# Kernel tuning notes

Hardware: AMD Instinct MI355X
Metric: run time of the kernel (lower is better)

Reference implementation:

```python
import jax, jax.numpy as jnp
import numpy as np

NUM_HEADS = 12

def rel_indices(N):
    # [N, N, 3] = (dx, dy, dist^2) between patches on an img x img grid
    img = int(N ** 0.5)
    ind = jnp.arange(img)[None, :] - jnp.arange(img)[:, None]      # [img, img]
    indx = jnp.tile(ind, (img, img))                               # [N, N]
    indy = jnp.repeat(jnp.repeat(ind, img, axis=0), img, axis=1)   # [N, N]
    indd = indx ** 2 + indy ** 2
    return jnp.stack([indx, indy, indd], axis=-1).astype(jnp.float32)

def setup_inputs() -> dict:
    key = jax.random.key(0)
    ks = jax.random.split(key, 8)
    B, N, C, H = 16, 576, 768, NUM_HEADS
    std = 0.02  # trunc_normal init scale in the original
    return {
        "x": jax.random.normal(ks[0], (B, N, C), jnp.float32),
        "w_qk": jax.random.normal(ks[1], (C, 2 * C), jnp.float32) * std,
        "w_v": jax.random.normal(ks[2], (C, C), jnp.float32) * std,
        "w_proj": jax.random.normal(ks[3], (C, C), jnp.float32) * std,
        "b_proj": jnp.zeros((C,), jnp.float32),
        "w_pos": jax.random.normal(ks[4], (3, H), jnp.float32) * std,
        "b_pos": jnp.zeros((H,), jnp.float32),
        "gating": jnp.ones((H,), jnp.float32),
    }

def reference(x, w_qk, w_v, w_proj, b_proj, w_pos, b_pos, gating):
    B, N, C = x.shape
    H = NUM_HEADS
    Dh = C // H
    scale = Dh ** -0.5

    # q, k: [B, H, N, Dh]
    qk = (x @ w_qk).reshape(B, N, 2, H, Dh)
    q = jnp.transpose(qk[:, :, 0], (0, 2, 1, 3))
    k = jnp.transpose(qk[:, :, 1], (0, 2, 1, 3))

    # content scores, softmax over keys
    patch_score = jax.nn.softmax(
        jnp.einsum("bhnd,bhmd->bhnm", q, k) * scale, axis=-1)

    # positional scores: rel_indices [N,N,3] -> [H,N,N], softmax over keys
    rel = rel_indices(N)
    pos_logits = jnp.einsum("nmk,kh->hnm", rel, w_pos) + b_pos[:, None, None]
    pos_score = jax.nn.softmax(pos_logits, axis=-1)  # [H, N, N]

    # sigmoid gating + renormalization
    g = jax.nn.sigmoid(gating)[None, :, None, None]
    attn = (1.0 - g) * patch_score + g * pos_score[None]
    attn = attn / jnp.sum(attn, axis=-1, keepdims=True)

    # v: [B, H, N, Dh]
    v = jnp.transpose((x @ w_v).reshape(B, N, H, Dh), (0, 2, 1, 3))

    out = jnp.einsum("bhnm,bhmd->bnhd", attn, v).reshape(B, N, C)
    out = out @ w_proj + b_proj
    return (out, attn, v)
```

## Files before the change

kernel.cpp:

```cpp
#include <hip/hip_runtime.h>
#include <hip/hip_bf16.h>

typedef __bf16 bf16;
typedef __attribute__((ext_vector_type(4))) __bf16 bf16x4;
typedef __attribute__((ext_vector_type(8))) __bf16 bf16x8;
typedef __attribute__((ext_vector_type(4))) float floatx4;

#define BB 16
#define NN 576
#define CC 768
#define HH 12
#define DH 64

#define GLOAD_LDS16(gp, lp) __builtin_amdgcn_global_load_lds( \
    (const __attribute__((address_space(1))) unsigned int*)(const void*)(gp), \
    (__attribute__((address_space(3))) unsigned int*)(void*)(lp), 16, 0, 0)

__global__ void k_convert(const float* __restrict__ in, bf16* __restrict__ out, int n4){
  int i = blockIdx.x*blockDim.x + threadIdx.x;
  if (i < n4){
    float4 f = ((const float4*)in)[i];
    bf16x4 o;
    o[0]=(bf16)f.x; o[1]=(bf16)f.y; o[2]=(bf16)f.z; o[3]=(bf16)f.w;
    ((bf16x4*)out)[i] = o;
  }
}

__global__ void k_transpose(const float* __restrict__ src, bf16* __restrict__ dst, int R, int Cc){
  __shared__ float tile[32][33];
  int c0 = blockIdx.x*32, r0 = blockIdx.y*32;
  int tx = threadIdx.x & 31, ty = threadIdx.x >> 5;
  #pragma unroll
  for (int i=0;i<4;i++)
    tile[ty + i*8][tx] = src[(size_t)(r0 + ty + i*8)*Cc + c0 + tx];
  __syncthreads();
  #pragma unroll
  for (int i=0;i<4;i++)
    dst[(size_t)(c0 + ty + i*8)*R + r0 + tx] = (bf16)tile[tx][ty + i*8];
}

__global__ __launch_bounds__(256) void k_pos(const float* __restrict__ w_pos, bf16* __restrict__ pos){
  int t = threadIdx.x, wv = t>>6, lane = t&63;
  int rowid = blockIdx.x*4 + wv;
  int h = rowid / NN, n = rowid % NN;
  float w0 = w_pos[h], w1 = w_pos[HH + h], w2 = w_pos[2*HH + h];
  int nx = n % 24, ny = n / 24;
  float e[9]; float mx = -1e30f;
  #pragma unroll
  for (int j=0;j<9;j++){
    int m = lane + 64*j;
    float dx = (float)(m % 24 - nx);
    float dy = (float)(m / 24 - ny);
    float l = dx*w0 + dy*w1 + (dx*dx + dy*dy)*w2;
    e[j] = l; mx = fmaxf(mx, l);
  }
  #pragma unroll
  for (int s=1;s<64;s<<=1) mx = fmaxf(mx, __shfl_xor(mx, s, 64));
  float sum = 0.f;
  #pragma unroll
  for (int j=0;j<9;j++){ e[j] = __expf(e[j]-mx); sum += e[j]; }
  #pragma unroll
  for (int s=1;s<64;s<<=1) sum += __shfl_xor(sum, s, 64);
  float inv = 1.f/sum;
  bf16* dst = pos + (size_t)rowid*NN;
  #pragma unroll
  for (int j=0;j<9;j++) dst[lane + 64*j] = (bf16)(e[j]*inv);
}

__device__ __forceinline__ void gemm128_main(
    const bf16* __restrict__ A, const bf16* __restrict__ B,
    int lda, int ldb, int K, bf16* As, bf16* Bs, floatx4 (*acc)[4])
{
  int t = threadIdx.x;
  int w = t>>6, m16 = t&15, q = (t&63)>>4;
  int wr = (w>>1)*64, wc = (w&1)*64;
  int sr = t>>2, kg = (t&3)*8;
  bf16* ldsA = As + w*512;
  bf16* ldsB = Bs + w*512;
  for (int k0 = 0; k0 < K; k0 += 32){
    GLOAD_LDS16(A + (size_t)sr*lda      + k0 + kg, ldsA);
    GLOAD_LDS16(A + (size_t)(sr+64)*lda + k0 + kg, ldsA + 2048);
    GLOAD_LDS16(B + (size_t)sr*ldb      + k0 + kg, ldsB);
    GLOAD_LDS16(B + (size_t)(sr+64)*ldb + k0 + kg, ldsB + 2048);
    __syncthreads();
    bf16x8 af[4], bfv[4];
    #pragma unroll
    for (int rt=0;rt<4;rt++) af[rt]  = *(const bf16x8*)&As[(wr + rt*16 + m16)*32 + q*8];
    #pragma unroll
    for (int ct=0;ct<4;ct++) bfv[ct] = *(const bf16x8*)&Bs[(wc + ct*16 + m16)*32 + q*8];
    #pragma unroll
    for (int rt=0;rt<4;rt++)
      #pragma unroll
      for (int ct=0;ct<4;ct++)
        acc[rt][ct] = __builtin_amdgcn_mfma_f32_16x16x32_bf16(af[rt], bfv[ct], acc[rt][ct], 0, 0, 0);
    __syncthreads();
  }
}

__global__ __launch_bounds__(256) void k_gemm1(
    const bf16* __restrict__ x_bf, const bf16* __restrict__ wcatT,
    bf16* __restrict__ q_bf, bf16* __restrict__ k_bf,
    bf16* __restrict__ vt_bf, float* __restrict__ v_out)
{
  __shared__ bf16 As[128*32];
  __shared__ bf16 Bs[128*32];
  int cb = blockIdx.x % 18, rb = blockIdx.x / 18;
  int rowBase = rb*128, colBase = cb*128;
  floatx4 zero = {0.f,0.f,0.f,0.f};
  floatx4 acc[4][4];
  #pragma unroll
  for (int a=0;a<4;a++)
    #pragma unroll
    for (int b=0;b<4;b++) acc[a][b] = zero;
  gemm128_main(x_bf + (size_t)rowBase*CC, wcatT + (size_t)colBase*CC, CC, CC, CC, As, Bs, acc);
  int t = threadIdx.x;
  int w = t>>6, m16 = t&15, q = (t&63)>>4;
  int wr = (w>>1)*64, wc = (w&1)*64;
  #pragma unroll
  for (int rt=0;rt<4;rt++){
    #pragma unroll
    for (int i=0;i<4;i++){
      int row = rowBase + wr + rt*16 + q*4 + i;
      int b = row / NN, n = row % NN;
      #pragma unroll
      for (int ct=0;ct<4;ct++){
        int col = colBase + wc + ct*16 + m16;
        float val = acc[rt][ct][i];
        if (col < 2*CC){
          int s = col / CC, rem = col % CC;
          int h = rem >> 6, d = rem & 63;
          bf16* dst = s ? k_bf : q_bf;
          float sv = s ? val : val*0.125f;
          dst[(((size_t)(b*HH + h)*NN + n) << 6) + d] = (bf16)sv;
        } else {
          int rem = col - 2*CC;
          int h = rem >> 6, d = rem & 63;
          v_out[(((size_t)(b*HH + h)*NN + n) << 6) + d] = val;
          vt_bf[((size_t)(b*HH + h)*DH + d)*NN + n] = (bf16)val;
        }
      }
    }
  }
}

__global__ __launch_bounds__(256, 2) void k_attn_pv(
    const bf16* __restrict__ q_bf, const bf16* __restrict__ k_bf,
    const bf16* __restrict__ vt_bf,
    const bf16* __restrict__ pos, const float* __restrict__ gating,
    float* __restrict__ attn_out, bf16* __restrict__ out1_bf)
{
  __shared__ __align__(16) char smem[64*1200];
  int qt = blockIdx.x % 9, bh = blockIdx.x / 9;
  int b = bh / HH, h = bh % HH;
  int n0 = qt*64;
  int t = threadIdx.x;
  int wv = t>>6, m16 = t&15, q = (t&63)>>4;

  const bf16* qrow = q_bf + ((size_t)bh*NN + n0 + wv*16 + m16)*DH;
  bf16x8 afr0 = *(const bf16x8*)&qrow[q*8];
  bf16x8 afr1 = *(const bf16x8*)&qrow[32 + q*8];

  const bf16* Kg = k_bf + (size_t)bh*NN*DH;
  floatx4 acc[36];
  #pragma unroll
  for (int T=0;T<36;T++) acc[T] = (floatx4){0.f,0.f,0.f,0.f};

  int key0 = t>>3, g16 = (t&7) ^ (key0 & 7);
  #pragma unroll
  for (int kt=0; kt<9; kt++){
    __syncthreads();
    const bf16* src0 = Kg + (size_t)(kt*64 + key0)*DH + g16*8;
    GLOAD_LDS16(src0,           smem + wv*1024);
    GLOAD_LDS16(src0 + 32*DH,   smem + 4096 + wv*1024);
    __syncthreads();
    #pragma unroll
    for (int ct=0; ct<4; ct++){
      int key = ct*16 + m16;
      int swz = key & 7;
      bf16x8 b0 = *(const bf16x8*)(smem + key*128 + ((q ^ swz)<<4));
      bf16x8 b1 = *(const bf16x8*)(smem + key*128 + (((4 + q) ^ swz)<<4));
      acc[kt*4+ct] = __builtin_amdgcn_mfma_f32_16x16x32_bf16(afr0, b0, acc[kt*4+ct], 0, 0, 0);
      acc[kt*4+ct] = __builtin_amdgcn_mfma_f32_16x16x32_bf16(afr1, b1, acc[kt*4+ct], 0, 0, 0);
    }
  }

  float mx[4], ps[4], bs[4];
  #pragma unroll
  for (int i=0;i<4;i++) mx[i] = -1e30f;
  #pragma unroll
  for (int T=0;T<36;T++)
    #pragma unroll
    for (int i=0;i<4;i++) mx[i] = fmaxf(mx[i], acc[T][i]);
  #pragma unroll
  for (int s=1;s<16;s<<=1)
    #pragma unroll
    for (int i=0;i<4;i++) mx[i] = fmaxf(mx[i], __shfl_xor(mx[i], s, 64));
  #pragma unroll
  for (int i=0;i<4;i++) ps[i] = 0.f;
  #pragma unroll
  for (int T=0;T<36;T++)
    #pragma unroll
    for (int i=0;i<4;i++){ float e = __expf(acc[T][i]-mx[i]); acc[T][i]=e; ps[i]+=e; }
  #pragma unroll
  for (int s=1;s<16;s<<=1)
    #pragma unroll
    for (int i=0;i<4;i++) ps[i] += __shfl_xor(ps[i], s, 64);

  float g = 1.f/(1.f + __expf(-gating[h]));
  float ig[4];
  #pragma unroll
  for (int i=0;i<4;i++){ ig[i] = (1.f-g)/ps[i]; bs[i] = 0.f; }

  int rowq = n0 + wv*16 + q*4;
  const bf16* posb = pos + ((size_t)h*NN + rowq)*NN + m16;
  #pragma unroll
  for (int T=0;T<36;T++)
    #pragma unroll
    for (int i=0;i<4;i++){
      float p = (float)posb[(size_t)i*NN + T*16];
      float a = ig[i]*acc[T][i] + g*p;
      acc[T][i] = a; bs[i] += a;
    }
  #pragma unroll
  for (int s=1;s<16;s<<=1)
    #pragma unroll
    for (int i=0;i<4;i++) bs[i] += __shfl_xor(bs[i], s, 64);
  float inv[4];
  #pragma unroll
  for (int i=0;i<4;i++) inv[i] = 1.f/bs[i];

  __syncthreads();
  float* arow = attn_out + ((size_t)bh*NN + rowq)*NN + m16;
  char* prow = smem + (size_t)(wv*16 + q*4)*1200 + m16*2;
  #pragma unroll
  for (int T=0;T<36;T++)
    #pragma unroll
    for (int i=0;i<4;i++){
      float a = acc[T][i]*inv[i];
      arow[(size_t)i*NN + T*16] = a;
      *(bf16*)(prow + i*1200 + T*32) = (bf16)a;
    }
  __syncthreads();

  floatx4 pacc[4];
  #pragma unroll
  for (int ct=0;ct<4;ct++) pacc[ct] = (floatx4){0.f,0.f,0.f,0.f};
  const char* pbase = smem + (size_t)(wv*16 + m16)*1200 + q*16;
  const bf16* vbase = vt_bf + (size_t)bh*DH*NN + q*8;
  #pragma unroll
  for (int c=0;c<18;c++){
    bf16x8 afr = *(const bf16x8*)(pbase + c*64);
    #pragma unroll
    for (int ct=0;ct<4;ct++){
      bf16x8 bfr = *(const bf16x8*)&vbase[(size_t)(ct*16+m16)*NN + c*32];
      pacc[ct] = __builtin_amdgcn_mfma_f32_16x16x32_bf16(afr, bfr, pacc[ct], 0, 0, 0);
    }
  }
  bf16* obase = out1_bf + ((size_t)(b*NN + rowq))*CC + h*DH + m16;
  #pragma unroll
  for (int ct=0;ct<4;ct++)
    #pragma unroll
    for (int i=0;i<4;i++)
      obase[(size_t)i*CC + ct*16] = (bf16)pacc[ct][i];
}

__global__ __launch_bounds__(256) void k_proj(
    const bf16* __restrict__ out1_bf, const bf16* __restrict__ wprojT,
    const float* __restrict__ b_proj, float* __restrict__ out)
{
  __shared__ bf16 As[128*32];
  __shared__ bf16 Bs[128*32];
  int cb = blockIdx.x % 6, rb = blockIdx.x / 6;
  int rowBase = rb*128, colBase = cb*128;
  floatx4 zero = {0.f,0.f,0.f,0.f};
  floatx4 acc[4][4];
  #pragma unroll
  for (int a=0;a<4;a++)
    #pragma unroll
    for (int b=0;b<4;b++) acc[a][b] = zero;
  gemm128_main(out1_bf + (size_t)rowBase*CC, wprojT + (size_t)colBase*CC, CC, CC, CC, As, Bs, acc);
  int t = threadIdx.x;
  int w = t>>6, m16 = t&15, q = (t&63)>>4;
  int wr = (w>>1)*64, wc = (w&1)*64;
  #pragma unroll
  for (int rt=0;rt<4;rt++){
    #pragma unroll
    for (int i=0;i<4;i++){
      int row = rowBase + wr + rt*16 + q*4 + i;
      #pragma unroll
      for (int ct=0;ct<4;ct++){
        int col = colBase + wc + ct*16 + m16;
        out[(size_t)row*CC + col] = acc[rt][ct][i] + b_proj[col];
      }
    }
  }
}

extern "C" void kernel_launch(void* const* d_in, const int* in_sizes, int n_in,
                              void* d_out, int out_size, void* d_ws, size_t ws_size,
                              hipStream_t stream)
{
  (void)in_sizes; (void)n_in; (void)out_size; (void)ws_size;
  const float* x      = (const float*)d_in[0];
  const float* w_qk   = (const float*)d_in[1];
  const float* w_v    = (const float*)d_in[2];
  const float* w_proj = (const float*)d_in[3];
  const float* b_proj = (const float*)d_in[4];
  const float* w_pos  = (const float*)d_in[5];
  const float* gating = (const float*)d_in[7];

  float* out_ptr  = (float*)d_out;
  float* attn_ptr = out_ptr + (size_t)BB*NN*CC;
  float* v_ptr    = attn_ptr + (size_t)BB*HH*NN*NN;

  char* w = (char*)d_ws;
  bf16* x_bf    = (bf16*)(w);
  bf16* wcatT   = (bf16*)(w + 14155776);
  bf16* wprojT  = (bf16*)(w + 17694720);
  bf16* q_bf    = (bf16*)(w + 18874368);
  bf16* k_bf    = (bf16*)(w + 33030144);
  bf16* vt_bf   = (bf16*)(w + 47185920);
  bf16* pos_bf  = (bf16*)(w + 61341696);
  bf16* out1_bf = x_bf;

  k_convert<<<6912, 256, 0, stream>>>(x, x_bf, (BB*NN*CC)/4);
  k_transpose<<<dim3(48,24), 256, 0, stream>>>(w_qk, wcatT, CC, 2*CC);
  k_transpose<<<dim3(24,24), 256, 0, stream>>>(w_v, wcatT + (size_t)2*CC*CC, CC, CC);
  k_transpose<<<dim3(24,24), 256, 0, stream>>>(w_proj, wprojT, CC, CC);
  k_pos<<<(HH*NN)/4, 256, 0, stream>>>(w_pos, pos_bf);
  k_gemm1<<<72*18, 256, 0, stream>>>(x_bf, wcatT, q_bf, k_bf, vt_bf, v_ptr);
  k_attn_pv<<<192*9, 256, 0, stream>>>(q_bf, k_bf, vt_bf, pos_bf, gating, attn_ptr, out1_bf);
  k_proj<<<72*6, 256, 0, stream>>>(out1_bf, wprojT, b_proj, out_ptr);
}
```

Before: 539.8 us.

## Transpose QK^T MFMA output so each lane owns a query row and stores vectorized

Swaps the MFMA operands so the score accumulator is transposed: each lane now holds four consecutive keys of a single query row. Softmax reductions become scalar per lane with only two cross-lane shuffles instead of per-element 4-step shuffles. The attn fp32 store becomes float4-wide and the LDS bf16 store 4-wide. The positional table is written in a permuted key order so each lane reads it with 16-byte loads. This adds a permuted layout coupling k_pos to the attention kernel's register mapping.

```diff
diff --git a/kernel.cpp b/kernel.cpp
--- a/kernel.cpp
+++ b/kernel.cpp
@@ -48,7 +48,10 @@
   float e[9]; float mx = -1e30f;
   #pragma unroll
   for (int j=0;j<9;j++){
-    int m = lane + 64*j;
+    int idx = lane + 64*j;
+    int qq = idx / 144;
+    int r  = idx - qq*144;
+    int m  = (r>>2)*16 + qq*4 + (r&3);
     float dx = (float)(m % 24 - nx);
     float dy = (float)(m / 24 - ny);
     float l = dx*w0 + dy*w1 + (dx*dx + dy*dy)*w2;
@@ -177,69 +180,58 @@
     for (int ct=0; ct<4; ct++){
       int key = ct*16 + m16;
       int swz = key & 7;
-      bf16x8 b0 = *(const bf16x8*)(smem + key*128 + ((q ^ swz)<<4));
-      bf16x8 b1 = *(const bf16x8*)(smem + key*128 + (((4 + q) ^ swz)<<4));
-      acc[kt*4+ct] = __builtin_amdgcn_mfma_f32_16x16x32_bf16(afr0, b0, acc[kt*4+ct], 0, 0, 0);
-      acc[kt*4+ct] = __builtin_amdgcn_mfma_f32_16x16x32_bf16(afr1, b1, acc[kt*4+ct], 0, 0, 0);
+      bf16x8 k0 = *(const bf16x8*)(smem + key*128 + ((q ^ swz)<<4));
+      bf16x8 k1 = *(const bf16x8*)(smem + key*128 + (((4 + q) ^ swz)<<4));
+      acc[kt*4+ct] = __builtin_amdgcn_mfma_f32_16x16x32_bf16(k0, afr0, acc[kt*4+ct], 0, 0, 0);
+      acc[kt*4+ct] = __builtin_amdgcn_mfma_f32_16x16x32_bf16(k1, afr1, acc[kt*4+ct], 0, 0, 0);
     }
   }
 
-  float mx[4], ps[4], bs[4];
-  #pragma unroll
-  for (int i=0;i<4;i++) mx[i] = -1e30f;
+  float mx = -1e30f;
   #pragma unroll
   for (int T=0;T<36;T++)
     #pragma unroll
-    for (int i=0;i<4;i++) mx[i] = fmaxf(mx[i], acc[T][i]);
-  #pragma unroll
-  for (int s=1;s<16;s<<=1)
-    #pragma unroll
-    for (int i=0;i<4;i++) mx[i] = fmaxf(mx[i], __shfl_xor(mx[i], s, 64));
-  #pragma unroll
-  for (int i=0;i<4;i++) ps[i] = 0.f;
+    for (int i=0;i<4;i++) mx = fmaxf(mx, acc[T][i]);
+  mx = fmaxf(mx, __shfl_xor(mx, 16, 64));
+  mx = fmaxf(mx, __shfl_xor(mx, 32, 64));
+  float ps = 0.f;
   #pragma unroll
   for (int T=0;T<36;T++)
     #pragma unroll
-    for (int i=0;i<4;i++){ float e = __expf(acc[T][i]-mx[i]); acc[T][i]=e; ps[i]+=e; }
-  #pragma unroll
-  for (int s=1;s<16;s<<=1)
-    #pragma unroll
-    for (int i=0;i<4;i++) ps[i] += __shfl_xor(ps[i], s, 64);
+    for (int i=0;i<4;i++){ float e = __expf(acc[T][i]-mx); acc[T][i]=e; ps += e; }
+  ps += __shfl_xor(ps, 16, 64);
+  ps += __shfl_xor(ps, 32, 64);
 
   float g = 1.f/(1.f + __expf(-gating[h]));
-  float ig[4];
-  #pragma unroll
-  for (int i=0;i<4;i++){ ig[i] = (1.f-g)/ps[i]; bs[i] = 0.f; }
-
-  int rowq = n0 + wv*16 + q*4;
-  const bf16* posb = pos + ((size_t)h*NN + rowq)*NN + m16;
-  #pragma unroll
-  for (int T=0;T<36;T++)
-    #pragma unroll
-    for (int i=0;i<4;i++){
-      float p = (float)posb[(size_t)i*NN + T*16];
-      float a = ig[i]*acc[T][i] + g*p;
-      acc[T][i] = a; bs[i] += a;
-    }
-  #pragma unroll
-  for (int s=1;s<16;s<<=1)
-    #pragma unroll
-    for (int i=0;i<4;i++) bs[i] += __shfl_xor(bs[i], s, 64);
-  float inv[4];
-  #pragma unroll
-  for (int i=0;i<4;i++) inv[i] = 1.f/bs[i];
+  float ig = (1.f-g)/ps, bs = 0.f;
+
+  const bf16* posrow = pos + ((size_t)h*NN + n0 + wv*16 + m16)*NN + q*144;
+  #pragma unroll
+  for (int T2=0;T2<18;T2++){
+    bf16x8 pv = *(const bf16x8*)&posrow[T2*8];
+    #pragma unroll
+    for (int u=0;u<2;u++)
+      #pragma unroll
+      for (int i=0;i<4;i++){
+        float a = ig*acc[T2*2+u][i] + g*(float)pv[u*4+i];
+        acc[T2*2+u][i] = a; bs += a;
+      }
+  }
+  bs += __shfl_xor(bs, 16, 64);
+  bs += __shfl_xor(bs, 32, 64);
+  float inv = 1.f/bs;
 
   __syncthreads();
-  float* arow = attn_out + ((size_t)bh*NN + rowq)*NN + m16;
-  char* prow = smem + (size_t)(wv*16 + q*4)*1200 + m16*2;
-  #pragma unroll
-  for (int T=0;T<36;T++)
-    #pragma unroll
-    for (int i=0;i<4;i++){
-      float a = acc[T][i]*inv[i];
-      arow[(size_t)i*NN + T*16] = a;
-      *(bf16*)(prow + i*1200 + T*32) = (bf16)a;
-    }
+  float* arow = attn_out + ((size_t)bh*NN + n0 + wv*16 + m16)*NN + q*4;
+  char* prow = smem + (size_t)(wv*16 + m16)*1200 + q*8;
+  #pragma unroll
+  for (int T=0;T<36;T++){
+    float4 o; bf16x4 pb;
+    o.x = acc[T][0]*inv; o.y = acc[T][1]*inv; o.z = acc[T][2]*inv; o.w = acc[T][3]*inv;
+    pb[0]=(bf16)o.x; pb[1]=(bf16)o.y; pb[2]=(bf16)o.z; pb[3]=(bf16)o.w;
+    *(float4*)(arow + (size_t)T*16) = o;
+    *(bf16x4*)(prow + T*32) = pb;
+  }
   __syncthreads();
 
   floatx4 pacc[4];
@@ -256,6 +248,7 @@
       pacc[ct] = __builtin_amdgcn_mfma_f32_16x16x32_bf16(afr, bfr, pacc[ct], 0, 0, 0);
     }
   }
+  int rowq = n0 + wv*16 + q*4;
   bf16* obase = out1_bf + ((size_t)(b*NN + rowq))*CC + h*DH + m16;
   #pragma unroll
   for (int ct=0;ct<4;ct++)
```

New measurement: 543.5 us. No clear change (+0.7%).
